# Performance work log

Measured on AMD Instinct MI355X. Metric: run time of the kernel, lower is better.

The kernel has to match this reference:

```python
import jax, jax.numpy as jnp
import numpy as np

N_NODES = 100000


def gcn_conv(x, src, dst, W, b, n_nodes):
    """PyG GCNConv: linear transform, add self-loops, sym-normalized scatter-add."""
    h = x @ W  # [N, out]
    loop = jnp.arange(n_nodes, dtype=src.dtype)
    s = jnp.concatenate([src, loop])
    d = jnp.concatenate([dst, loop])
    ones = jnp.ones(s.shape[0], dtype=h.dtype)
    deg = jax.ops.segment_sum(ones, d, num_segments=n_nodes)  # in-degree incl self-loops
    dinv = jnp.where(deg > 0, jax.lax.rsqrt(deg), 0.0)
    norm = dinv[s] * dinv[d]  # [E+N]
    msg = h[s] * norm[:, None]  # gather + scale
    out = jax.ops.segment_sum(msg, d, num_segments=n_nodes)  # scatter-add
    return out + b


def setup_inputs() -> dict:
    key = jax.random.key(0)
    k1, k2, k3, k4, k5, k6 = jax.random.split(key, 6)
    x = jax.random.normal(k1, (N_NODES, 128), dtype=jnp.float32)
    edge_index = jax.random.randint(k2, (2, 1600000), 0, N_NODES, dtype=jnp.int64)
    W1 = jax.random.normal(k3, (128, 32), dtype=jnp.float32) * (1.0 / np.sqrt(128))
    b1 = jax.random.normal(k4, (32,), dtype=jnp.float32) * 0.01
    W2 = jax.random.normal(k5, (32, 1), dtype=jnp.float32) * (1.0 / np.sqrt(32))
    b2 = jax.random.normal(k6, (1,), dtype=jnp.float32) * 0.01
    return {"x": x, "edge_index": edge_index, "W1": W1, "b1": b1, "W2": W2, "b2": b2}


def reference(x, edge_index, W1, b1, W2, b2):
    n = x.shape[0]
    src, dst = edge_index[0], edge_index[1]
    h = gcn_conv(x, src, dst, W1, b1, n)
    h = jax.nn.relu(h)
    h = gcn_conv(h, src, dst, W2, b2, n)  # [N, 1]
    return jnp.mean(h, axis=0)  # [1]
```

## Files before the change

### kernel.cpp

```cpp
#include <hip/hip_runtime.h>

constexpr int FIN = 128;
constexpr int FH  = 32;
constexpr int NBSHIFT = 8;
constexpr int BKN = 1 << NBSHIFT;
constexpr int MAXNB = 512;
constexpr int CAP = 6144;
constexpr int SRC_BITS = 18;
constexpr unsigned SRC_MASK = (1u << SRC_BITS) - 1;
constexpr int GSTRIDE = 16;

typedef int int4v __attribute__((ext_vector_type(4)));

#if defined(__has_builtin)
#if __has_builtin(__builtin_amdgcn_cvt_pk_f32_fp8) && __has_builtin(__builtin_amdgcn_cvt_pk_fp8_f32)
#define HAVE_HW_FP8 1
#endif
#endif

__device__ __forceinline__ unsigned char f32_to_e4m3(float f) {
    unsigned u = __float_as_uint(f);
    unsigned sgn = (u >> 24) & 0x80u;
    unsigned a = u & 0x7FFFFFFFu;
    if (a < 0x3A800000u) return (unsigned char)sgn;
    if (a < 0x3C800000u) {
        int m = __float2int_rn(__uint_as_float(a) * 512.0f);
        return (unsigned char)(sgn | (unsigned)m);
    }
    unsigned r = a + 0x7FFFFu + ((a >> 20) & 1u);
    unsigned e8 = r >> 23;
    unsigned em = ((e8 - 120u) << 3) | ((r >> 20) & 7u);
    if (em > 0x7Eu) em = 0x7Eu;
    return (unsigned char)(sgn | em);
}

__device__ __forceinline__ unsigned pack_fp8x4(float a0, float a1, float a2, float a3) {
#ifdef HAVE_HW_FP8
    unsigned v = __builtin_amdgcn_cvt_pk_fp8_f32(a0, a1, 0u, false);
    v = __builtin_amdgcn_cvt_pk_fp8_f32(a2, a3, v, true);
    return v;
#else
    return (unsigned)f32_to_e4m3(a0) | ((unsigned)f32_to_e4m3(a1) << 8)
         | ((unsigned)f32_to_e4m3(a2) << 16) | ((unsigned)f32_to_e4m3(a3) << 24);
#endif
}

__device__ __forceinline__ float e4m3_to_f32(unsigned b) {
    unsigned em = b & 0x7Fu;
    float mag = (em >= 8u) ? __uint_as_float((em + 960u) << 20)
                           : (float)em * 0.001953125f;
    return __uint_as_float(__float_as_uint(mag) | ((b & 0x80u) << 24));
}

__device__ __forceinline__ void unpack_fp8x4(unsigned u, float& f0, float& f1, float& f2, float& f3) {
#ifdef HAVE_HW_FP8
    typedef __attribute__((ext_vector_type(2))) float f32x2;
    f32x2 lo = __builtin_amdgcn_cvt_pk_f32_fp8(u, false);
    f32x2 hi = __builtin_amdgcn_cvt_pk_f32_fp8(u, true);
    f0 = lo.x; f1 = lo.y; f2 = hi.x; f3 = hi.y;
#else
    f0 = e4m3_to_f32(u & 0xFFu);
    f1 = e4m3_to_f32((u >> 8) & 0xFFu);
    f2 = e4m3_to_f32((u >> 16) & 0xFFu);
    f3 = e4m3_to_f32(u >> 24);
#endif
}

__global__ __launch_bounds__(512) void k_binA(const int* __restrict__ src, const int* __restrict__ dst,
                                              int* __restrict__ gcur, unsigned* __restrict__ gbin,
                                              int E, int NB, int chunk) {
    __shared__ int hist[MAXNB];
    __shared__ int base[MAXNB];
    __shared__ int lcur[MAXNB];
    int t = threadIdx.x;
    int beg = blockIdx.x * chunk;
    int end = min(beg + chunk, E);
    if (beg >= E) return;
    for (int b = t; b < NB; b += blockDim.x) hist[b] = 0;
    __syncthreads();
    for (int i = beg + t; i < end; i += blockDim.x)
        atomicAdd(&hist[((unsigned)dst[i]) >> NBSHIFT], 1);
    __syncthreads();
    for (int b = t; b < NB; b += blockDim.x) {
        int h = hist[b];
        base[b] = h ? atomicAdd(&gcur[b * GSTRIDE], h) : 0;
        lcur[b] = 0;
    }
    __syncthreads();
    for (int i = beg + t; i < end; i += blockDim.x) {
        int d = dst[i];
        int s = src[i];
        int b = ((unsigned)d) >> NBSHIFT;
        int pos = atomicAdd(&lcur[b], 1);
        int idx = base[b] + pos;
        if (idx < CAP)
            gbin[(size_t)b * CAP + idx] = ((unsigned)(d & (BKN - 1)) << SRC_BITS) | (unsigned)s;
    }
}

__global__ __launch_bounds__(512) void k_b1deg(const int* __restrict__ gcur, const unsigned* __restrict__ gbin,
                        float* __restrict__ ndf, int* __restrict__ degb, int N) {
    __shared__ int deg[BKN];
    int t = threadIdx.x;
    int b = blockIdx.x;
    if (t < BKN) deg[t] = 0;
    __syncthreads();
    int len = min(gcur[b * GSTRIDE], CAP);
    const unsigned* eb = gbin + (size_t)b * CAP;
    for (int i = t; i < len; i += blockDim.x)
        atomicAdd(&deg[eb[i] >> SRC_BITS], 1);
    __syncthreads();
    if (t < BKN) {
        int g = (b << NBSHIFT) + t;
        if (g < N) {
            ndf[2 * (size_t)g] = rsqrtf((float)deg[t] + 1.0f);
            degb[g] = deg[t];
        }
    }
}

__global__ __launch_bounds__(256) void k_gemm1(const float* __restrict__ x, const float* __restrict__ W1,
                        const float* __restrict__ ndf, unsigned char* __restrict__ h1s, int N) {
    __shared__ float Wl[FIN * 33];
    int t = threadIdx.x;
    for (int i = t; i < FIN * FH; i += 256) {
        int k = i >> 5, f = i & 31;
        Wl[k * 33 + f] = W1[i];
    }
    __syncthreads();
    int gid = blockIdx.x * 256 + t;
    int row = gid >> 2;
    int l4 = t & 3;
    if (row >= N) return;
    const float4* xr = (const float4*)(x + (size_t)row * FIN);
    const float* wb = Wl + l4 * 8;
    float a0 = 0.f, a1 = 0.f, a2 = 0.f, a3 = 0.f, a4 = 0.f, a5 = 0.f, a6 = 0.f, a7 = 0.f;
    for (int k4 = 0; k4 < FIN / 4; k4++) {
        float4 xv = xr[k4];
        const float* w0 = wb + (k4 * 4) * 33;
#pragma unroll
        for (int j = 0; j < 4; j++) {
            const float* w = w0 + j * 33;
            float xs = (j == 0) ? xv.x : (j == 1) ? xv.y : (j == 2) ? xv.z : xv.w;
            a0 += xs * w[0]; a1 += xs * w[1]; a2 += xs * w[2]; a3 += xs * w[3];
            a4 += xs * w[4]; a5 += xs * w[5]; a6 += xs * w[6]; a7 += xs * w[7];
        }
    }
    float dv = ndf[2 * (size_t)row];
    unsigned up0 = pack_fp8x4(dv * a0, dv * a1, dv * a2, dv * a3);
    unsigned up1 = pack_fp8x4(dv * a4, dv * a5, dv * a6, dv * a7);
    uint2* hr = (uint2*)(h1s + (size_t)row * FH) + l4;
    *hr = make_uint2(up0, up1);
}

__global__ __launch_bounds__(512) void k_sortg(const int* __restrict__ gcur, const unsigned* __restrict__ gbin,
                                               const int* __restrict__ degb, float* __restrict__ ndf,
                                               const unsigned char* __restrict__ h1s,
                                               const float* __restrict__ b1, const float* __restrict__ W2,
                                               float* __restrict__ partials, int N) {
    __shared__ unsigned sorted[CAP];
    __shared__ int deg[BKN];
    __shared__ int off[BKN];
    __shared__ int cur[BKN];
    int t = threadIdx.x;
    int b = blockIdx.x;
    if (t < BKN) {
        int g = (b << NBSHIFT) + t;
        deg[t] = (g < N) ? degb[g] : 0;
        cur[t] = deg[t];
    }
    __syncthreads();
    for (int o = 1; o < BKN; o <<= 1) {
        int v = 0;
        if (t < BKN && t >= o) v = cur[t - o];
        __syncthreads();
        if (t < BKN) cur[t] += v;
        __syncthreads();
    }
    if (t < BKN) {
        off[t] = cur[t] - deg[t];
        cur[t] = cur[t] - deg[t];
    }
    __syncthreads();
    int len = min(gcur[b * GSTRIDE], CAP);
    const unsigned* eb = gbin + (size_t)b * CAP;
    for (int i = t; i < len; i += blockDim.x) {
        unsigned ent = eb[i];
        int dl = (int)(ent >> SRC_BITS);
        int pos = atomicAdd(&cur[dl], 1);
        if (pos < CAP) sorted[pos] = ent & SRC_MASK;
    }
    __syncthreads();
    int l8 = t & 7;
    float wavepart = 0.0f;
    for (int nb = 0; nb < BKN; nb += 64) {
        int dl = nb + (t >> 3);
        int g = (b << NBSHIFT) + dl;
        if (g < N) {
            float dv = ndf[2 * (size_t)g];
            int dgg = deg[dl];
            int beg = off[dl];
            float a0 = 0.f, a1 = 0.f, a2 = 0.f, a3 = 0.f;
            int e = 0;
            for (; e + 4 <= dgg; e += 4) {
                int s0 = sorted[beg + e];
                int s1 = sorted[beg + e + 1];
                int s2 = sorted[beg + e + 2];
                int s3 = sorted[beg + e + 3];
                unsigned u0 = *((const unsigned*)(h1s + (size_t)s0 * FH) + l8);
                unsigned u1 = *((const unsigned*)(h1s + (size_t)s1 * FH) + l8);
                unsigned u2 = *((const unsigned*)(h1s + (size_t)s2 * FH) + l8);
                unsigned u3 = *((const unsigned*)(h1s + (size_t)s3 * FH) + l8);
                float f0, f1, f2, f3;
                unpack_fp8x4(u0, f0, f1, f2, f3); a0 += f0; a1 += f1; a2 += f2; a3 += f3;
                unpack_fp8x4(u1, f0, f1, f2, f3); a0 += f0; a1 += f1; a2 += f2; a3 += f3;
                unpack_fp8x4(u2, f0, f1, f2, f3); a0 += f0; a1 += f1; a2 += f2; a3 += f3;
                unpack_fp8x4(u3, f0, f1, f2, f3); a0 += f0; a1 += f1; a2 += f2; a3 += f3;
            }
            for (; e < dgg; e++) {
                int s = sorted[beg + e];
                unsigned u = *((const unsigned*)(h1s + (size_t)s * FH) + l8);
                float f0, f1, f2, f3;
                unpack_fp8x4(u, f0, f1, f2, f3); a0 += f0; a1 += f1; a2 += f2; a3 += f3;
            }
            unsigned uh = *((const unsigned*)(h1s + (size_t)g * FH) + l8);
            float h0, h1f, h2, h3;
            unpack_fp8x4(uh, h0, h1f, h2, h3);
            float4 b4 = *(const float4*)(b1 + l8 * 4);
            float4 w4 = *(const float4*)(W2 + l8 * 4);
            float z0 = fmaxf(dv * (a0 + h0) + b4.x, 0.0f);
            float z1 = fmaxf(dv * (a1 + h1f) + b4.y, 0.0f);
            float z2 = fmaxf(dv * (a2 + h2) + b4.z, 0.0f);
            float z3 = fmaxf(dv * (a3 + h3) + b4.w, 0.0f);
            float yv = z0 * w4.x + z1 * w4.y + z2 * w4.z + z3 * w4.w;
            yv += __shfl_xor(yv, 1);
            yv += __shfl_xor(yv, 2);
            yv += __shfl_xor(yv, 4);
            if (l8 == 0) {
                float ys = dv * yv;
                ndf[2 * (size_t)g + 1] = ys;
                wavepart += dv * ys;
            }
        }
    }
#pragma unroll
    for (int o = 32; o > 0; o >>= 1) wavepart += __shfl_down(wavepart, o);
    if ((t & 63) == 0) partials[b * 8 + (t >> 6)] = wavepart;
}

__global__ void k_edge2(const int* __restrict__ src, const int* __restrict__ dst,
                        const float* __restrict__ ndf, float* __restrict__ partials, int E) {
    int i = blockIdx.x * blockDim.x + threadIdx.x;
    int base = i * 8;
    float p = 0.0f;
    if (base + 8 <= E) {
        int4v sA = __builtin_nontemporal_load((const int4v*)(src + base));
        int4v sB = __builtin_nontemporal_load((const int4v*)(src + base + 4));
        int4v dA = __builtin_nontemporal_load((const int4v*)(dst + base));
        int4v dB = __builtin_nontemporal_load((const int4v*)(dst + base + 4));
        float2 vs0 = *(const float2*)(ndf + 2 * (size_t)sA.x);
        float2 vs1 = *(const float2*)(ndf + 2 * (size_t)sA.y);
        float2 vs2 = *(const float2*)(ndf + 2 * (size_t)sA.z);
        float2 vs3 = *(const float2*)(ndf + 2 * (size_t)sA.w);
        float2 vs4 = *(const float2*)(ndf + 2 * (size_t)sB.x);
        float2 vs5 = *(const float2*)(ndf + 2 * (size_t)sB.y);
        float2 vs6 = *(const float2*)(ndf + 2 * (size_t)sB.z);
        float2 vs7 = *(const float2*)(ndf + 2 * (size_t)sB.w);
        float2 vd0 = *(const float2*)(ndf + 2 * (size_t)dA.x);
        float2 vd1 = *(const float2*)(ndf + 2 * (size_t)dA.y);
        float2 vd2 = *(const float2*)(ndf + 2 * (size_t)dA.z);
        float2 vd3 = *(const float2*)(ndf + 2 * (size_t)dA.w);
        float2 vd4 = *(const float2*)(ndf + 2 * (size_t)dB.x);
        float2 vd5 = *(const float2*)(ndf + 2 * (size_t)dB.y);
        float2 vd6 = *(const float2*)(ndf + 2 * (size_t)dB.z);
        float2 vd7 = *(const float2*)(ndf + 2 * (size_t)dB.w);
        p  = vs0.y * vd0.x + vs1.y * vd1.x + vs2.y * vd2.x + vs3.y * vd3.x;
        p += vs4.y * vd4.x + vs5.y * vd5.x + vs6.y * vd6.x + vs7.y * vd7.x;
    } else if (base < E) {
        for (int j = base; j < E; j++) {
            float2 vs = *(const float2*)(ndf + 2 * (size_t)src[j]);
            float2 vd = *(const float2*)(ndf + 2 * (size_t)dst[j]);
            p += vs.y * vd.x;
        }
    }
#pragma unroll
    for (int off = 32; off > 0; off >>= 1) p += __shfl_down(p, off);
    if ((threadIdx.x & 63) == 0) partials[(blockIdx.x * blockDim.x + threadIdx.x) >> 6] = p;
}

__global__ void k_out(const float* __restrict__ partials, int nP,
                      const float* __restrict__ b2, float* __restrict__ out, int N) {
    __shared__ float red[1024];
    int t = threadIdx.x;
    float s = 0.0f;
    for (int i = t; i < nP; i += 1024) s += partials[i];
    red[t] = s;
    __syncthreads();
    for (int off = 512; off > 0; off >>= 1) {
        if (t < off) red[t] += red[t + off];
        __syncthreads();
    }
    if (t == 0) out[0] = red[0] * (1.0f / (float)N) + b2[0];
}

extern "C" void kernel_launch(void* const* d_in, const int* in_sizes, int n_in,
                              void* d_out, int out_size, void* d_ws, size_t ws_size,
                              hipStream_t stream) {
    const float* x   = (const float*)d_in[0];
    const int*   ei  = (const int*)d_in[1];
    const float* W1  = (const float*)d_in[2];
    const float* b1  = (const float*)d_in[3];
    const float* W2  = (const float*)d_in[4];
    const float* b2  = (const float*)d_in[5];
    float*       out = (float*)d_out;

    int N = in_sizes[0] / FIN;
    int E = in_sizes[1] / 2;
    const int* src = ei;
    const int* dst = ei + E;

    int NB = (N + BKN - 1) >> NBSHIFT;

    int thr = 256;
    int blkG1 = (N * 4 + thr - 1) / thr;
    int blkE8 = ((E + 7) / 8 + thr - 1) / thr;
    int ablk  = 512;
    int chunk = (E + ablk - 1) / ablk;

    int nWB2 = NB * 8;
    int nWE  = blkE8 * (thr / 64);
    int nP   = nWB2 + nWE;

    char* w = (char*)d_ws;
    int*           gcur  = (int*)w;            w += (size_t)NB * GSTRIDE * 4;
    float*         ndf   = (float*)w;          w += (size_t)N * 8;
    int*           degb  = (int*)w;            w += (size_t)N * 4;
    float*         parts = (float*)w;          w += (((size_t)nP * 4 + 255) & ~(size_t)255);
    unsigned*      gbin  = (unsigned*)w;       w += (size_t)NB * CAP * 4;
    unsigned char* h1s   = (unsigned char*)w;

    (void)hipMemsetAsync(gcur, 0, (size_t)NB * GSTRIDE * 4, stream);

    k_binA<<<dim3(ablk), dim3(512), 0, stream>>>(src, dst, gcur, gbin, E, NB, chunk);
    k_b1deg<<<dim3(NB), dim3(512), 0, stream>>>(gcur, gbin, ndf, degb, N);
    k_gemm1<<<dim3(blkG1), dim3(thr), 0, stream>>>(x, W1, ndf, h1s, N);
    k_sortg<<<dim3(NB), dim3(512), 0, stream>>>(gcur, gbin, degb, ndf, h1s, b1, W2, parts, N);
    k_edge2<<<dim3(blkE8), dim3(thr), 0, stream>>>(src, dst, ndf, parts + nWB2, E);
    k_out<<<dim3(1), dim3(1024), 0, stream>>>(parts, nP, b2, out, N);
}
```

Before: 120.5 us.

## Split destination bins across two blocks and compute layer-2 edges from binned lists

Each 256-node destination bin is now handled by two blocks, each owning half of the nodes. That doubles the grid for the degree and gather kernels, from about 391 to about 782 blocks, so more of the GPU is busy. The layer-2 edge reduction now reads the packed binned edge list and keeps the destination dinv in shared memory. Before, it streamed the raw src/dst arrays and did two random ndf gathers per edge. In exchange, each half-block rereads the full bin and filters out half the entries, and the sort kernel's shared buffer shrinks to 3072 entries, which could overflow for skewed bins.

```diff
diff --git a/kernel.cpp b/kernel.cpp
--- a/kernel.cpp
+++ b/kernel.cpp
@@ -4,8 +4,10 @@
 constexpr int FH  = 32;
 constexpr int NBSHIFT = 8;
 constexpr int BKN = 1 << NBSHIFT;
+constexpr int HKN = BKN / 2;
 constexpr int MAXNB = 512;
 constexpr int CAP = 6144;
+constexpr int HCAP = 3072;
 constexpr int SRC_BITS = 18;
 constexpr unsigned SRC_MASK = (1u << SRC_BITS) - 1;
 constexpr int GSTRIDE = 16;
@@ -100,18 +102,21 @@
 
 __global__ __launch_bounds__(512) void k_b1deg(const int* __restrict__ gcur, const unsigned* __restrict__ gbin,
                         float* __restrict__ ndf, int* __restrict__ degb, int N) {
-    __shared__ int deg[BKN];
-    int t = threadIdx.x;
-    int b = blockIdx.x;
-    if (t < BKN) deg[t] = 0;
+    __shared__ int deg[HKN];
+    int t = threadIdx.x;
+    int b2 = blockIdx.x;
+    int b = b2 >> 1, half = b2 & 1;
+    if (t < HKN) deg[t] = 0;
     __syncthreads();
     int len = min(gcur[b * GSTRIDE], CAP);
     const unsigned* eb = gbin + (size_t)b * CAP;
-    for (int i = t; i < len; i += blockDim.x)
-        atomicAdd(&deg[eb[i] >> SRC_BITS], 1);
-    __syncthreads();
-    if (t < BKN) {
-        int g = (b << NBSHIFT) + t;
+    for (int i = t; i < len; i += blockDim.x) {
+        int dl = (int)(eb[i] >> SRC_BITS);
+        if ((dl >> 7) == half) atomicAdd(&deg[dl & (HKN - 1)], 1);
+    }
+    __syncthreads();
+    if (t < HKN) {
+        int g = (b << NBSHIFT) + half * HKN + t;
         if (g < N) {
             ndf[2 * (size_t)g] = rsqrtf((float)deg[t] + 1.0f);
             degb[g] = deg[t];
@@ -158,26 +163,28 @@
                                                const unsigned char* __restrict__ h1s,
                                                const float* __restrict__ b1, const float* __restrict__ W2,
                                                float* __restrict__ partials, int N) {
-    __shared__ unsigned sorted[CAP];
-    __shared__ int deg[BKN];
-    __shared__ int off[BKN];
-    __shared__ int cur[BKN];
-    int t = threadIdx.x;
-    int b = blockIdx.x;
-    if (t < BKN) {
-        int g = (b << NBSHIFT) + t;
+    __shared__ unsigned sorted[HCAP];
+    __shared__ int deg[HKN];
+    __shared__ int off[HKN];
+    __shared__ int cur[HKN];
+    int t = threadIdx.x;
+    int b2 = blockIdx.x;
+    int b = b2 >> 1, half = b2 & 1;
+    int gbase = (b << NBSHIFT) + half * HKN;
+    if (t < HKN) {
+        int g = gbase + t;
         deg[t] = (g < N) ? degb[g] : 0;
         cur[t] = deg[t];
     }
     __syncthreads();
-    for (int o = 1; o < BKN; o <<= 1) {
+    for (int o = 1; o < HKN; o <<= 1) {
         int v = 0;
-        if (t < BKN && t >= o) v = cur[t - o];
+        if (t < HKN && t >= o) v = cur[t - o];
         __syncthreads();
-        if (t < BKN) cur[t] += v;
+        if (t < HKN) cur[t] += v;
         __syncthreads();
     }
-    if (t < BKN) {
+    if (t < HKN) {
         off[t] = cur[t] - deg[t];
         cur[t] = cur[t] - deg[t];
     }
@@ -187,15 +194,17 @@
     for (int i = t; i < len; i += blockDim.x) {
         unsigned ent = eb[i];
         int dl = (int)(ent >> SRC_BITS);
-        int pos = atomicAdd(&cur[dl], 1);
-        if (pos < CAP) sorted[pos] = ent & SRC_MASK;
+        if ((dl >> 7) == half) {
+            int pos = atomicAdd(&cur[dl & (HKN - 1)], 1);
+            if (pos < HCAP) sorted[pos] = ent & SRC_MASK;
+        }
     }
     __syncthreads();
     int l8 = t & 7;
     float wavepart = 0.0f;
-    for (int nb = 0; nb < BKN; nb += 64) {
+    for (int nb = 0; nb < HKN; nb += 64) {
         int dl = nb + (t >> 3);
-        int g = (b << NBSHIFT) + dl;
+        int g = gbase + dl;
         if (g < N) {
             float dv = ndf[2 * (size_t)g];
             int dgg = deg[dl];
@@ -245,47 +254,36 @@
     }
 #pragma unroll
     for (int o = 32; o > 0; o >>= 1) wavepart += __shfl_down(wavepart, o);
-    if ((t & 63) == 0) partials[b * 8 + (t >> 6)] = wavepart;
-}
-
-__global__ void k_edge2(const int* __restrict__ src, const int* __restrict__ dst,
-                        const float* __restrict__ ndf, float* __restrict__ partials, int E) {
-    int i = blockIdx.x * blockDim.x + threadIdx.x;
-    int base = i * 8;
+    if ((t & 63) == 0) partials[b2 * 8 + (t >> 6)] = wavepart;
+}
+
+__global__ __launch_bounds__(512) void k_edge2b(const int* __restrict__ gcur, const unsigned* __restrict__ gbin,
+                                                const float* __restrict__ ndf,
+                                                float* __restrict__ partials, int N) {
+    __shared__ float dinvl[HKN];
+    int t = threadIdx.x;
+    int b2 = blockIdx.x;
+    int b = b2 >> 1, half = b2 & 1;
+    int gbase = (b << NBSHIFT) + half * HKN;
+    if (t < HKN) {
+        int g = gbase + t;
+        dinvl[t] = (g < N) ? ndf[2 * (size_t)g] : 0.0f;
+    }
+    __syncthreads();
+    int len = min(gcur[b * GSTRIDE], CAP);
+    const unsigned* eb = gbin + (size_t)b * CAP;
     float p = 0.0f;
-    if (base + 8 <= E) {
-        int4v sA = __builtin_nontemporal_load((const int4v*)(src + base));
-        int4v sB = __builtin_nontemporal_load((const int4v*)(src + base + 4));
-        int4v dA = __builtin_nontemporal_load((const int4v*)(dst + base));
-        int4v dB = __builtin_nontemporal_load((const int4v*)(dst + base + 4));
-        float2 vs0 = *(const float2*)(ndf + 2 * (size_t)sA.x);
-        float2 vs1 = *(const float2*)(ndf + 2 * (size_t)sA.y);
-        float2 vs2 = *(const float2*)(ndf + 2 * (size_t)sA.z);
-        float2 vs3 = *(const float2*)(ndf + 2 * (size_t)sA.w);
-        float2 vs4 = *(const float2*)(ndf + 2 * (size_t)sB.x);
-        float2 vs5 = *(const float2*)(ndf + 2 * (size_t)sB.y);
-        float2 vs6 = *(const float2*)(ndf + 2 * (size_t)sB.z);
-        float2 vs7 = *(const float2*)(ndf + 2 * (size_t)sB.w);
-        float2 vd0 = *(const float2*)(ndf + 2 * (size_t)dA.x);
-        float2 vd1 = *(const float2*)(ndf + 2 * (size_t)dA.y);
-        float2 vd2 = *(const float2*)(ndf + 2 * (size_t)dA.z);
-        float2 vd3 = *(const float2*)(ndf + 2 * (size_t)dA.w);
-        float2 vd4 = *(const float2*)(ndf + 2 * (size_t)dB.x);
-        float2 vd5 = *(const float2*)(ndf + 2 * (size_t)dB.y);
-        float2 vd6 = *(const float2*)(ndf + 2 * (size_t)dB.z);
-        float2 vd7 = *(const float2*)(ndf + 2 * (size_t)dB.w);
-        p  = vs0.y * vd0.x + vs1.y * vd1.x + vs2.y * vd2.x + vs3.y * vd3.x;
-        p += vs4.y * vd4.x + vs5.y * vd5.x + vs6.y * vd6.x + vs7.y * vd7.x;
-    } else if (base < E) {
-        for (int j = base; j < E; j++) {
-            float2 vs = *(const float2*)(ndf + 2 * (size_t)src[j]);
-            float2 vd = *(const float2*)(ndf + 2 * (size_t)dst[j]);
-            p += vs.y * vd.x;
+    for (int i = t; i < len; i += blockDim.x) {
+        unsigned ent = eb[i];
+        int dl = (int)(ent >> SRC_BITS);
+        if ((dl >> 7) == half) {
+            int s = (int)(ent & SRC_MASK);
+            p += ndf[2 * (size_t)s + 1] * dinvl[dl & (HKN - 1)];
         }
     }
 #pragma unroll
-    for (int off = 32; off > 0; off >>= 1) p += __shfl_down(p, off);
-    if ((threadIdx.x & 63) == 0) partials[(blockIdx.x * blockDim.x + threadIdx.x) >> 6] = p;
+    for (int o = 32; o > 0; o >>= 1) p += __shfl_down(p, o);
+    if ((t & 63) == 0) partials[b2 * 8 + (t >> 6)] = p;
 }
 
 __global__ void k_out(const float* __restrict__ partials, int nP,
@@ -320,15 +318,15 @@
     const int* dst = ei + E;
 
     int NB = (N + BKN - 1) >> NBSHIFT;
+    int NB2 = NB * 2;
 
     int thr = 256;
     int blkG1 = (N * 4 + thr - 1) / thr;
-    int blkE8 = ((E + 7) / 8 + thr - 1) / thr;
     int ablk  = 512;
     int chunk = (E + ablk - 1) / ablk;
 
-    int nWB2 = NB * 8;
-    int nWE  = blkE8 * (thr / 64);
+    int nWB2 = NB2 * 8;
+    int nWE  = NB2 * 8;
     int nP   = nWB2 + nWE;
 
     char* w = (char*)d_ws;
@@ -342,9 +340,9 @@
     (void)hipMemsetAsync(gcur, 0, (size_t)NB * GSTRIDE * 4, stream);
 
     k_binA<<<dim3(ablk), dim3(512), 0, stream>>>(src, dst, gcur, gbin, E, NB, chunk);
-    k_b1deg<<<dim3(NB), dim3(512), 0, stream>>>(gcur, gbin, ndf, degb, N);
+    k_b1deg<<<dim3(NB2), dim3(512), 0, stream>>>(gcur, gbin, ndf, degb, N);
     k_gemm1<<<dim3(blkG1), dim3(thr), 0, stream>>>(x, W1, ndf, h1s, N);
-    k_sortg<<<dim3(NB), dim3(512), 0, stream>>>(gcur, gbin, degb, ndf, h1s, b1, W2, parts, N);
-    k_edge2<<<dim3(blkE8), dim3(thr), 0, stream>>>(src, dst, ndf, parts + nWB2, E);
+    k_sortg<<<dim3(NB2), dim3(512), 0, stream>>>(gcur, gbin, degb, ndf, h1s, b1, W2, parts, N);
+    k_edge2b<<<dim3(NB2), dim3(512), 0, stream>>>(gcur, gbin, ndf, parts + nWB2, N);
     k_out<<<dim3(1), dim3(1024), 0, stream>>>(parts, nP, b2, out, N);
 }
```

Result: faster. 103.0 us (median of 2 runs) (-14.5%).

## Reuse destination-binned edges for layer-2 pass and halve bucket size

Applied to the files above, without the earlier changes.

The layer-2 edge reduction now walks the packed, destination-binned edge list already built for layer 1, instead of reading raw src/dst. Each block caches its bucket's destination dinv values in shared memory, so only the source value is a random global gather. This halves index traffic and removes one random gather per edge. Buckets also shrink from 256 to 128 nodes, with capacity halved and the max bucket count doubled, so the sort/gather and binning kernels run more, smaller blocks, at the cost of more histogram entries in binning.

```diff
diff --git a/kernel.cpp b/kernel.cpp
--- a/kernel.cpp
+++ b/kernel.cpp
@@ -2,10 +2,10 @@
 
 constexpr int FIN = 128;
 constexpr int FH  = 32;
-constexpr int NBSHIFT = 8;
-constexpr int BKN = 1 << NBSHIFT;
-constexpr int MAXNB = 512;
-constexpr int CAP = 6144;
+constexpr int BSHIFT = 7;
+constexpr int BKN = 1 << BSHIFT;
+constexpr int MAXNB = 1024;
+constexpr int CAP = 3072;
 constexpr int SRC_BITS = 18;
 constexpr unsigned SRC_MASK = (1u << SRC_BITS) - 1;
 constexpr int GSTRIDE = 16;
@@ -79,7 +79,7 @@
     for (int b = t; b < NB; b += blockDim.x) hist[b] = 0;
     __syncthreads();
     for (int i = beg + t; i < end; i += blockDim.x)
-        atomicAdd(&hist[((unsigned)dst[i]) >> NBSHIFT], 1);
+        atomicAdd(&hist[((unsigned)dst[i]) >> BSHIFT], 1);
     __syncthreads();
     for (int b = t; b < NB; b += blockDim.x) {
         int h = hist[b];
@@ -90,7 +90,7 @@
     for (int i = beg + t; i < end; i += blockDim.x) {
         int d = dst[i];
         int s = src[i];
-        int b = ((unsigned)d) >> NBSHIFT;
+        int b = ((unsigned)d) >> BSHIFT;
         int pos = atomicAdd(&lcur[b], 1);
         int idx = base[b] + pos;
         if (idx < CAP)
@@ -111,7 +111,7 @@
         atomicAdd(&deg[eb[i] >> SRC_BITS], 1);
     __syncthreads();
     if (t < BKN) {
-        int g = (b << NBSHIFT) + t;
+        int g = (b << BSHIFT) + t;
         if (g < N) {
             ndf[2 * (size_t)g] = rsqrtf((float)deg[t] + 1.0f);
             degb[g] = deg[t];
@@ -164,8 +164,9 @@
     __shared__ int cur[BKN];
     int t = threadIdx.x;
     int b = blockIdx.x;
+    int gbase = b << BSHIFT;
     if (t < BKN) {
-        int g = (b << NBSHIFT) + t;
+        int g = gbase + t;
         deg[t] = (g < N) ? degb[g] : 0;
         cur[t] = deg[t];
     }
@@ -195,7 +196,7 @@
     float wavepart = 0.0f;
     for (int nb = 0; nb < BKN; nb += 64) {
         int dl = nb + (t >> 3);
-        int g = (b << NBSHIFT) + dl;
+        int g = gbase + dl;
         if (g < N) {
             float dv = ndf[2 * (size_t)g];
             int dgg = deg[dl];
@@ -248,44 +249,29 @@
     if ((t & 63) == 0) partials[b * 8 + (t >> 6)] = wavepart;
 }
 
-__global__ void k_edge2(const int* __restrict__ src, const int* __restrict__ dst,
-                        const float* __restrict__ ndf, float* __restrict__ partials, int E) {
-    int i = blockIdx.x * blockDim.x + threadIdx.x;
-    int base = i * 8;
+__global__ __launch_bounds__(512) void k_edge2b(const int* __restrict__ gcur, const unsigned* __restrict__ gbin,
+                                                const float* __restrict__ ndf,
+                                                float* __restrict__ partials, int N) {
+    __shared__ float dinvl[BKN];
+    int t = threadIdx.x;
+    int b = blockIdx.x;
+    int gbase = b << BSHIFT;
+    if (t < BKN) {
+        int g = gbase + t;
+        dinvl[t] = (g < N) ? ndf[2 * (size_t)g] : 0.0f;
+    }
+    __syncthreads();
+    int len = min(gcur[b * GSTRIDE], CAP);
+    const unsigned* eb = gbin + (size_t)b * CAP;
     float p = 0.0f;
-    if (base + 8 <= E) {
-        int4v sA = __builtin_nontemporal_load((const int4v*)(src + base));
-        int4v sB = __builtin_nontemporal_load((const int4v*)(src + base + 4));
-        int4v dA = __builtin_nontemporal_load((const int4v*)(dst + base));
-        int4v dB = __builtin_nontemporal_load((const int4v*)(dst + base + 4));
-        float2 vs0 = *(const float2*)(ndf + 2 * (size_t)sA.x);
-        float2 vs1 = *(const float2*)(ndf + 2 * (size_t)sA.y);
-        float2 vs2 = *(const float2*)(ndf + 2 * (size_t)sA.z);
-        float2 vs3 = *(const float2*)(ndf + 2 * (size_t)sA.w);
-        float2 vs4 = *(const float2*)(ndf + 2 * (size_t)sB.x);
-        float2 vs5 = *(const float2*)(ndf + 2 * (size_t)sB.y);
-        float2 vs6 = *(const float2*)(ndf + 2 * (size_t)sB.z);
-        float2 vs7 = *(const float2*)(ndf + 2 * (size_t)sB.w);
-        float2 vd0 = *(const float2*)(ndf + 2 * (size_t)dA.x);
-        float2 vd1 = *(const float2*)(ndf + 2 * (size_t)dA.y);
-        float2 vd2 = *(const float2*)(ndf + 2 * (size_t)dA.z);
-        float2 vd3 = *(const float2*)(ndf + 2 * (size_t)dA.w);
-        float2 vd4 = *(const float2*)(ndf + 2 * (size_t)dB.x);
-        float2 vd5 = *(const float2*)(ndf + 2 * (size_t)dB.y);
-        float2 vd6 = *(const float2*)(ndf + 2 * (size_t)dB.z);
-        float2 vd7 = *(const float2*)(ndf + 2 * (size_t)dB.w);
-        p  = vs0.y * vd0.x + vs1.y * vd1.x + vs2.y * vd2.x + vs3.y * vd3.x;
-        p += vs4.y * vd4.x + vs5.y * vd5.x + vs6.y * vd6.x + vs7.y * vd7.x;
-    } else if (base < E) {
-        for (int j = base; j < E; j++) {
-            float2 vs = *(const float2*)(ndf + 2 * (size_t)src[j]);
-            float2 vd = *(const float2*)(ndf + 2 * (size_t)dst[j]);
-            p += vs.y * vd.x;
-        }
+    for (int i = t; i < len; i += blockDim.x) {
+        unsigned ent = eb[i];
+        int s = (int)(ent & SRC_MASK);
+        p += ndf[2 * (size_t)s + 1] * dinvl[ent >> SRC_BITS];
     }
 #pragma unroll
-    for (int off = 32; off > 0; off >>= 1) p += __shfl_down(p, off);
-    if ((threadIdx.x & 63) == 0) partials[(blockIdx.x * blockDim.x + threadIdx.x) >> 6] = p;
+    for (int o = 32; o > 0; o >>= 1) p += __shfl_down(p, o);
+    if ((t & 63) == 0) partials[b * 8 + (t >> 6)] = p;
 }
 
 __global__ void k_out(const float* __restrict__ partials, int nP,
@@ -319,17 +305,16 @@
     const int* src = ei;
     const int* dst = ei + E;
 
-    int NB = (N + BKN - 1) >> NBSHIFT;
+    int NB = (N + BKN - 1) >> BSHIFT;
 
     int thr = 256;
     int blkG1 = (N * 4 + thr - 1) / thr;
-    int blkE8 = ((E + 7) / 8 + thr - 1) / thr;
     int ablk  = 512;
     int chunk = (E + ablk - 1) / ablk;
 
-    int nWB2 = NB * 8;
-    int nWE  = blkE8 * (thr / 64);
-    int nP   = nWB2 + nWE;
+    int nWS = NB * 8;
+    int nWE = NB * 8;
+    int nP  = nWS + nWE;
 
     char* w = (char*)d_ws;
     int*           gcur  = (int*)w;            w += (size_t)NB * GSTRIDE * 4;
@@ -345,6 +330,6 @@
     k_b1deg<<<dim3(NB), dim3(512), 0, stream>>>(gcur, gbin, ndf, degb, N);
     k_gemm1<<<dim3(blkG1), dim3(thr), 0, stream>>>(x, W1, ndf, h1s, N);
     k_sortg<<<dim3(NB), dim3(512), 0, stream>>>(gcur, gbin, degb, ndf, h1s, b1, W2, parts, N);
-    k_edge2<<<dim3(blkE8), dim3(thr), 0, stream>>>(src, dst, ndf, parts + nWB2, E);
+    k_edge2b<<<dim3(NB), dim3(512), 0, stream>>>(gcur, gbin, ndf, parts + nWS, N);
     k_out<<<dim3(1), dim3(1024), 0, stream>>>(parts, nP, b2, out, N);
 }
```

Result: faster. 109.3 us (-9.3%).
